# Performance work log

Measured on AMD Instinct MI355X. Metric: run time of the kernel, lower is better.

Reference implementation:

```python
import jax, jax.numpy as jnp
import numpy as np

DIM = 256
NUM_HEADS = 8
CHUNK = 64
EPS = 1e-5


def layernorm(x, g, b):
    m = jnp.mean(x, axis=-1, keepdims=True)
    v = jnp.mean((x - m) ** 2, axis=-1, keepdims=True)
    return (x - m) / jnp.sqrt(v + EPS) * g + b


def setup_inputs() -> dict:
    key = jax.random.key(0)
    ks = jax.random.split(key, 12)
    B, C, H, W = 8, DIM, 64, 64
    s = 1.0 / np.sqrt(C)
    return {
        "x": jax.random.normal(ks[0], (B, C, H, W), jnp.float32),
        "CVA_input": jax.random.normal(ks[1], (B, C, H, W), jnp.float32),
        "qn_g": jnp.ones((C,), jnp.float32), "qn_b": jnp.zeros((C,), jnp.float32),
        "kn_g": jnp.ones((C,), jnp.float32), "kn_b": jnp.zeros((C,), jnp.float32),
        "vn_g": jnp.ones((C,), jnp.float32), "vn_b": jnp.zeros((C,), jnp.float32),
        "Wq": jax.random.normal(ks[2], (C, C), jnp.float32) * s,
        "bq": jnp.zeros((C,), jnp.float32),
        "Wk": jax.random.normal(ks[3], (C, C), jnp.float32) * s,
        "bk": jnp.zeros((C,), jnp.float32),
        "Wv": jax.random.normal(ks[4], (C, C), jnp.float32) * s,
        "bv": jnp.zeros((C,), jnp.float32),
        "Wp": jax.random.normal(ks[5], (C, C), jnp.float32) * s,
        "bp": jnp.zeros((C,), jnp.float32),
    }


def reference(x, CVA_input, qn_g, qn_b, kn_g, kn_b, vn_g, vn_b,
              Wq, bq, Wk, bk, Wv, bv, Wp, bp):
    B, C, H, W = x.shape
    N = H * W
    nh = NUM_HEADS
    hd = C // nh
    scale = hd ** -0.5
    nc = N // CHUNK  # number of non-overlapping chunks

    xs = x.reshape(B, C, N).transpose(0, 2, 1)          # [B,N,C]
    cva = CVA_input.reshape(B, -1, C)                    # [B,N,C] (raw reshape, as in torch)

    def heads(t):  # [B,N,C] -> [B,nh,nc,CHUNK,hd]
        return t.reshape(B, N, nh, hd).transpose(0, 2, 1, 3).reshape(B, nh, nc, CHUNK, hd)

    q = heads(layernorm(cva, qn_g, qn_b) @ Wq + bq)
    k = heads(layernorm(cva, kn_g, kn_b) @ Wk + bk)
    v = heads(layernorm(xs, vn_g, vn_b) @ Wv + bv)

    # block-local attention: each chunk attends only within itself
    scores = jnp.einsum('bhncd,bhnkd->bhnck', q, k) * scale  # [B,nh,nc,CHUNK,CHUNK]
    probs = jax.nn.softmax(scores, axis=-1)
    o = jnp.einsum('bhnck,bhnkd->bhncd', probs, v)           # [B,nh,nc,CHUNK,hd]

    o = o.reshape(B, nh, N, hd).transpose(0, 2, 1, 3).reshape(B, N, C)
    out = o @ Wp + bp                                        # [B,N,C]
    return out.transpose(0, 2, 1).reshape(B, C, H, W)
```

## Files before the change

kernel.cpp:

```cpp
#include <hip/hip_runtime.h>
#include <hip/hip_bf16.h>

#define NTOK 4096
#define BATCH 8
#define NROWS (BATCH * NTOK)

typedef __attribute__((ext_vector_type(8))) short bfx8;
typedef __attribute__((ext_vector_type(4))) short bfx4;
typedef __attribute__((ext_vector_type(4))) float f32x4;

__device__ __forceinline__ short f2bf(float f) {
    unsigned u = __builtin_bit_cast(unsigned, f);
    u += 0x7fffu + ((u >> 16) & 1u);
    return (short)(u >> 16);
}
__device__ __forceinline__ unsigned pk2(float a, float b) {
    return (unsigned)(unsigned short)f2bf(a) | ((unsigned)(unsigned short)f2bf(b) << 16);
}

#define MFMA16(a, b, c) __builtin_amdgcn_mfma_f32_16x16x32_bf16(a, b, c, 0, 0, 0)
#define LGKM0()                                              \
    do {                                                     \
        asm volatile("s_waitcnt lgkmcnt(0)" ::: "memory");   \
        __builtin_amdgcn_sched_barrier(0);                   \
    } while (0)

__global__ __launch_bounds__(256) void prep_w(
    const float* __restrict__ Wq, const float* __restrict__ Wk,
    const float* __restrict__ Wv, const float* __restrict__ Wp,
    const float* __restrict__ qg, const float* __restrict__ qb,
    const float* __restrict__ kg, const float* __restrict__ kb,
    const float* __restrict__ vg, const float* __restrict__ vb,
    short* __restrict__ wt, float* __restrict__ bbp) {
    int m = blockIdx.x;
    int ci0 = blockIdx.y * 16;
    const float *W, *g, *be;
    float scale = 1.0f;
    if (m == 0)      { W = Wq; g = qg; be = qb; scale = 0.17677669529663687f; }
    else if (m == 1) { W = Wk; g = kg; be = kb; }
    else if (m == 2) { W = Wv; g = vg; be = vb; }
    else             { W = Wp; g = nullptr; be = nullptr; }
    __shared__ float tile[16][257];
    int t = threadIdx.x;
#pragma unroll
    for (int i = 0; i < 16; i++)
        tile[i][t] = W[(size_t)(ci0 + i) * 256 + t];
    __syncthreads();
    float p = 0.f;
    if (be) {
#pragma unroll
        for (int i = 0; i < 16; i++) p += be[ci0 + i] * tile[i][t];
    }
    bbp[(m * 16 + blockIdx.y) * 256 + t] = p;
    short* WT = wt + m * 65536 + t * 256 + ci0;
    bfx8 o0, o1;
#pragma unroll
    for (int j = 0; j < 8; j++) {
        float gv = g ? g[ci0 + j] : 1.0f;
        o0[j] = f2bf(scale * gv * tile[j][t]);
    }
#pragma unroll
    for (int j = 0; j < 8; j++) {
        float gv = g ? g[ci0 + 8 + j] : 1.0f;
        o1[j] = f2bf(scale * gv * tile[8 + j][t]);
    }
    *reinterpret_cast<bfx8*>(WT) = o0;
    *reinterpret_cast<bfx8*>(WT + 8) = o1;
}

__global__ __launch_bounds__(256) void prep_b(
    const float* __restrict__ bq, const float* __restrict__ bk,
    const float* __restrict__ bv, const float* __restrict__ bp,
    const float* __restrict__ bbp, float* __restrict__ bb) {
    int m = blockIdx.x, t = threadIdx.x;
    const float* bias = (m == 0) ? bq : (m == 1) ? bk : (m == 2) ? bv : bp;
    float scale = (m == 0) ? 0.17677669529663687f : 1.0f;
    float s = bias[t];
#pragma unroll
    for (int i = 0; i < 16; i++) s += bbp[(m * 16 + i) * 256 + t];
    bb[m * 256 + t] = scale * s;
}

__global__ __launch_bounds__(512, 4) void mega(const float* __restrict__ x,
                                               const float* __restrict__ cva,
                                               const short* __restrict__ wt,
                                               const float* __restrict__ bb,
                                               float* __restrict__ out) {
    int id = blockIdx.x;
    int b = id >> 6, ch = id & 63;
    int t = threadIdx.x, w = t >> 6, l = t & 63, c = l & 15, g = l >> 4;

    __shared__ short A[64 * 264];
    __shared__ short scr_[8][2560];
    __shared__ float red[8][64][2];
    short* S = scr_[w];

    const float* xb   = x + (size_t)b * 1048576 + ch * 64;
    const float* cvab = cva + (size_t)(b * 4096 + ch * 64) * 256;

    {
        float4 vv[8];
#pragma unroll
        for (int i = 0; i < 8; i++)
            vv[i] = *reinterpret_cast<const float4*>(cvab + (size_t)(w * 8 + i) * 256 + l * 4);
#pragma unroll
        for (int i = 0; i < 8; i++) {
            int row = w * 8 + i;
            float4 v = vv[i];
            float s = v.x + v.y + v.z + v.w;
            float q2 = v.x * v.x + v.y * v.y + v.z * v.z + v.w * v.w;
#pragma unroll
            for (int m = 1; m < 64; m <<= 1) { s += __shfl_xor(s, m); q2 += __shfl_xor(q2, m); }
            float mean = s * (1.0f / 256.0f);
            float rstd = rsqrtf(q2 * (1.0f / 256.0f) - mean * mean + 1e-5f);
            bfx4 o;
            o[0] = f2bf((v.x - mean) * rstd);
            o[1] = f2bf((v.y - mean) * rstd);
            o[2] = f2bf((v.z - mean) * rstd);
            o[3] = f2bf((v.w - mean) * rstd);
            *reinterpret_cast<bfx4*>(A + row * 264 + l * 4) = o;
        }
    }
    __syncthreads();

    f32x4 qa[4][2] = {}, ka[4][2] = {};
    {
        const short* wq0 = wt + (size_t)(w * 32 + c) * 256 + g * 8;
        const short* wq1 = wq0 + 16 * 256;
        const short* wk0 = wq0 + 65536;
        const short* wk1 = wq1 + 65536;
#pragma unroll
        for (int ks = 0; ks < 8; ks++) {
            bfx8 af[4];
#pragma unroll
            for (int m = 0; m < 4; m++)
                af[m] = *reinterpret_cast<const bfx8*>(A + (m * 16 + c) * 264 + ks * 32 + g * 8);
            bfx8 q0 = *reinterpret_cast<const bfx8*>(wq0 + ks * 32);
            bfx8 q1 = *reinterpret_cast<const bfx8*>(wq1 + ks * 32);
            bfx8 k0 = *reinterpret_cast<const bfx8*>(wk0 + ks * 32);
            bfx8 k1 = *reinterpret_cast<const bfx8*>(wk1 + ks * 32);
#pragma unroll
            for (int m = 0; m < 4; m++) {
                qa[m][0] = MFMA16(af[m], q0, qa[m][0]);
                qa[m][1] = MFMA16(af[m], q1, qa[m][1]);
                ka[m][0] = MFMA16(af[m], k0, ka[m][0]);
                ka[m][1] = MFMA16(af[m], k1, ka[m][1]);
            }
        }
    }

    float xg[32];
#pragma unroll
    for (int i = 0; i < 32; i++) xg[i] = xb[(size_t)(w * 32 + i) * 4096 + l];

    bfx8 qf[4];
    {
        float b0 = bb[w * 32 + c], b1 = bb[w * 32 + 16 + c];
#pragma unroll
        for (int m = 0; m < 4; m++)
#pragma unroll
            for (int j = 0; j < 4; j++) {
                S[(m * 16 + g * 4 + j) * 40 + c]      = f2bf(qa[m][0][j] + b0);
                S[(m * 16 + g * 4 + j) * 40 + 16 + c] = f2bf(qa[m][1][j] + b1);
            }
        LGKM0();
#pragma unroll
        for (int np = 0; np < 4; np++)
            qf[np] = *reinterpret_cast<const bfx8*>(S + (np * 16 + c) * 40 + g * 8);
        LGKM0();
    }

    bfx8 kf[4];
    {
        float b0 = bb[256 + w * 32 + c], b1 = bb[256 + w * 32 + 16 + c];
#pragma unroll
        for (int m = 0; m < 4; m++)
#pragma unroll
            for (int j = 0; j < 4; j++) {
                S[(m * 16 + g * 4 + j) * 40 + c]      = f2bf(ka[m][0][j] + b0);
                S[(m * 16 + g * 4 + j) * 40 + 16 + c] = f2bf(ka[m][1][j] + b1);
            }
        LGKM0();
#pragma unroll
        for (int m = 0; m < 4; m++)
            kf[m] = *reinterpret_cast<const bfx8*>(S + (m * 16 + c) * 40 + g * 8);
        LGKM0();
    }

    {
        float s = 0.f, q2 = 0.f;
#pragma unroll
        for (int i = 0; i < 32; i++) { s += xg[i]; q2 += xg[i] * xg[i]; }
        red[w][l][0] = s;
        red[w][l][1] = q2;
    }
    __syncthreads();

    float xmean, xrstd;
    {
        float s = 0.f, q2 = 0.f;
#pragma unroll
        for (int j2 = 0; j2 < 8; j2++) { s += red[j2][l][0]; q2 += red[j2][l][1]; }
        xmean = s * (1.0f / 256.0f);
        xrstd = rsqrtf(q2 * (1.0f / 256.0f) - xmean * xmean + 1e-5f);
    }

#pragma unroll
    for (int i2 = 0; i2 < 4; i2++) {
        bfx8 o;
#pragma unroll
        for (int jj = 0; jj < 8; jj++) o[jj] = f2bf((xg[i2 * 8 + jj] - xmean) * xrstd);
        *reinterpret_cast<bfx8*>(A + l * 264 + w * 32 + i2 * 8) = o;
    }
    __syncthreads();

    f32x4 va[4][2] = {};
    {
        const short* w0 = wt + 2 * 65536 + (size_t)(w * 32 + c) * 256 + g * 8;
        const short* w1 = w0 + 16 * 256;
#pragma unroll
        for (int ks = 0; ks < 8; ks++) {
            bfx8 af[4];
#pragma unroll
            for (int m = 0; m < 4; m++)
                af[m] = *reinterpret_cast<const bfx8*>(A + (m * 16 + c) * 264 + ks * 32 + g * 8);
            bfx8 v0 = *reinterpret_cast<const bfx8*>(w0 + ks * 32);
            bfx8 v1 = *reinterpret_cast<const bfx8*>(w1 + ks * 32);
#pragma unroll
            for (int m = 0; m < 4; m++) {
                va[m][0] = MFMA16(af[m], v0, va[m][0]);
                va[m][1] = MFMA16(af[m], v1, va[m][1]);
            }
        }
    }

    f32x4 sa[4][4] = {};
#pragma unroll
    for (int m = 0; m < 4; m++)
#pragma unroll
        for (int np = 0; np < 4; np++)
            sa[m][np] = MFMA16(kf[m], qf[np], sa[m][np]);

    float rs[4];
#pragma unroll
    for (int np = 0; np < 4; np++) {
        float mx = sa[0][np][0];
#pragma unroll
        for (int m = 0; m < 4; m++)
#pragma unroll
            for (int j = 0; j < 4; j++) mx = fmaxf(mx, sa[m][np][j]);
        mx = fmaxf(mx, __shfl_xor(mx, 16));
        mx = fmaxf(mx, __shfl_xor(mx, 32));
        float sum = 0.f;
#pragma unroll
        for (int m = 0; m < 4; m++)
#pragma unroll
            for (int j = 0; j < 4; j++) {
                float e = __expf(sa[m][np][j] - mx);
                sa[m][np][j] = e;
                sum += e;
            }
        sum += __shfl_xor(sum, 16);
        sum += __shfl_xor(sum, 32);
        rs[np] = 1.0f / sum;
    }

    unsigned Pp[4][4][2];
#pragma unroll
    for (int m = 0; m < 4; m++)
#pragma unroll
        for (int np = 0; np < 4; np++) {
            Pp[m][np][0] = pk2(sa[m][np][0], sa[m][np][1]);
            Pp[m][np][1] = pk2(sa[m][np][2], sa[m][np][3]);
        }
    __syncthreads();

    bfx8 vf[2][2];
    {
        float b0 = bb[512 + w * 32 + c], b1 = bb[512 + w * 32 + 16 + c];
#pragma unroll
        for (int m = 0; m < 4; m++) {
            bfx4 t0, t1;
#pragma unroll
            for (int j = 0; j < 4; j++) {
                t0[j] = f2bf(va[m][0][j] + b0);
                t1[j] = f2bf(va[m][1][j] + b1);
            }
            *reinterpret_cast<bfx4*>(S + c * 72 + m * 16 + g * 4)        = t0;
            *reinterpret_cast<bfx4*>(S + (16 + c) * 72 + m * 16 + g * 4) = t1;
        }
        LGKM0();
#pragma unroll
        for (int ks = 0; ks < 2; ks++)
#pragma unroll
            for (int mD = 0; mD < 2; mD++)
                vf[ks][mD] = *reinterpret_cast<const bfx8*>(S + (mD * 16 + c) * 72 + ks * 32 + g * 8);
        LGKM0();
    }

    f32x4 oa[2][4] = {};
#pragma unroll
    for (int ks = 0; ks < 2; ks++) {
#pragma unroll
        for (int m2 = 0; m2 < 2; m2++)
#pragma unroll
            for (int np = 0; np < 4; np++) {
                *reinterpret_cast<unsigned*>(S + (np * 16 + c) * 40 + m2 * 16 + g * 4)     = Pp[ks * 2 + m2][np][0];
                *reinterpret_cast<unsigned*>(S + (np * 16 + c) * 40 + m2 * 16 + g * 4 + 2) = Pp[ks * 2 + m2][np][1];
            }
        LGKM0();
        bfx8 pf[4];
#pragma unroll
        for (int np = 0; np < 4; np++)
            pf[np] = *reinterpret_cast<const bfx8*>(S + (np * 16 + c) * 40 + g * 8);
        LGKM0();
#pragma unroll
        for (int mD = 0; mD < 2; mD++)
#pragma unroll
            for (int np = 0; np < 4; np++)
                oa[mD][np] = MFMA16(vf[ks][mD], pf[np], oa[mD][np]);
    }

#pragma unroll
    for (int mD = 0; mD < 2; mD++)
#pragma unroll
        for (int np = 0; np < 4; np++) {
            bfx4 o4;
#pragma unroll
            for (int j = 0; j < 4; j++) o4[j] = f2bf(oa[mD][np][j] * rs[np]);
            *reinterpret_cast<bfx4*>(A + (np * 16 + c) * 264 + w * 32 + mD * 16 + g * 4) = o4;
        }
    __syncthreads();

    {
        f32x4 pa[4][2] = {};
        const short* w0 = wt + 3 * 65536 + (size_t)(w * 32 + c) * 256 + g * 8;
        const short* w1 = w0 + 16 * 256;
#pragma unroll
        for (int ks = 0; ks < 8; ks++) {
            bfx8 af[4];
#pragma unroll
            for (int m = 0; m < 4; m++)
                af[m] = *reinterpret_cast<const bfx8*>(A + (m * 16 + c) * 264 + ks * 32 + g * 8);
            bfx8 p0 = *reinterpret_cast<const bfx8*>(w0 + ks * 32);
            bfx8 p1 = *reinterpret_cast<const bfx8*>(w1 + ks * 32);
#pragma unroll
            for (int m = 0; m < 4; m++) {
                pa[m][0] = MFMA16(af[m], p0, pa[m][0]);
                pa[m][1] = MFMA16(af[m], p1, pa[m][1]);
            }
        }
        float* trw = reinterpret_cast<float*>(S);
        float* outb = out + (size_t)b * 1048576 + ch * 64;
#pragma unroll
        for (int p = 0; p < 2; p++) {
            float bvv = bb[768 + w * 32 + p * 16 + c];
#pragma unroll
            for (int m = 0; m < 4; m++)
#pragma unroll
                for (int j = 0; j < 4; j++)
                    trw[c * 65 + m * 16 + g * 4 + j] = pa[m][p][j] + bvv;
            LGKM0();
#pragma unroll
            for (int cl = 0; cl < 16; cl++) {
                int co = w * 32 + p * 16 + cl;
                outb[(size_t)co * 4096 + l] = trw[cl * 65 + l];
            }
            LGKM0();
        }
    }
}

extern "C" void kernel_launch(void* const* d_in, const int* in_sizes, int n_in,
                              void* d_out, int out_size, void* d_ws, size_t ws_size,
                              hipStream_t stream) {
    const float* x   = (const float*)d_in[0];
    const float* cva = (const float*)d_in[1];
    const float* qg  = (const float*)d_in[2];
    const float* qb  = (const float*)d_in[3];
    const float* kg  = (const float*)d_in[4];
    const float* kb  = (const float*)d_in[5];
    const float* vg  = (const float*)d_in[6];
    const float* vb  = (const float*)d_in[7];
    const float* Wq  = (const float*)d_in[8];
    const float* bq  = (const float*)d_in[9];
    const float* Wk  = (const float*)d_in[10];
    const float* bk  = (const float*)d_in[11];
    const float* Wv  = (const float*)d_in[12];
    const float* bv  = (const float*)d_in[13];
    const float* Wp  = (const float*)d_in[14];
    const float* bp  = (const float*)d_in[15];
    float* out = (float*)d_out;
    char* ws = (char*)d_ws;

    short* wt  = (short*)(ws);
    float* bb  = (float*)(ws + 4 * 65536 * sizeof(short));
    float* bbp = bb + 1024;

    prep_w<<<dim3(4, 16), 256, 0, stream>>>(Wq, Wk, Wv, Wp, qg, qb, kg, kb, vg, vb,
                                            wt, bbp);
    prep_b<<<4, 256, 0, stream>>>(bq, bk, bv, bp, bbp, bb);

    mega<<<512, 512, 0, stream>>>(x, cva, wt, bb, out);
}
```

Baseline: 70.92 us.

## Restructure cva LayerNorm loads, hoist softmax before V GEMM, store output directly

The cva LayerNorm now has each lane load 16 contiguous floats of a row, with four rows per wavefront reduced over 16 lanes, so the shuffle reduction is shorter and LDS writes are wider. The QK^T scores and softmax move ahead of the V projection GEMM, which may let the exp work overlap with the MFMA stream. The final projection drops its LDS transpose and writes float4 stores straight from the MFMA accumulator layout, removing LDS traffic and two waits. The direct stores are 16-byte segments spread across channels rather than fully coalesced 256-byte rows, and holding more values live may raise register pressure.

Result: faster. 67.08 us (-5.4%).

```diff
diff --git a/kernel.cpp b/kernel.cpp
--- a/kernel.cpp
+++ b/kernel.cpp
@@ -99,26 +99,44 @@
     const float* cvab = cva + (size_t)(b * 4096 + ch * 64) * 256;
 
     {
-        float4 vv[8];
-#pragma unroll
-        for (int i = 0; i < 8; i++)
-            vv[i] = *reinterpret_cast<const float4*>(cvab + (size_t)(w * 8 + i) * 256 + l * 4);
-#pragma unroll
-        for (int i = 0; i < 8; i++) {
-            int row = w * 8 + i;
-            float4 v = vv[i];
-            float s = v.x + v.y + v.z + v.w;
-            float q2 = v.x * v.x + v.y * v.y + v.z * v.z + v.w * v.w;
-#pragma unroll
-            for (int m = 1; m < 64; m <<= 1) { s += __shfl_xor(s, m); q2 += __shfl_xor(q2, m); }
+        int r16 = l >> 4;
+        float fv[2][16];
+#pragma unroll
+        for (int p2 = 0; p2 < 2; p2++) {
+            int row = w * 8 + p2 * 4 + r16;
+#pragma unroll
+            for (int i = 0; i < 4; i++) {
+                float4 v4 = *reinterpret_cast<const float4*>(
+                    cvab + (size_t)row * 256 + c * 16 + i * 4);
+                fv[p2][i * 4 + 0] = v4.x;
+                fv[p2][i * 4 + 1] = v4.y;
+                fv[p2][i * 4 + 2] = v4.z;
+                fv[p2][i * 4 + 3] = v4.w;
+            }
+        }
+#pragma unroll
+        for (int p2 = 0; p2 < 2; p2++) {
+            int row = w * 8 + p2 * 4 + r16;
+            float s = 0.f, q2 = 0.f;
+#pragma unroll
+            for (int i = 0; i < 16; i++) {
+                s += fv[p2][i];
+                q2 += fv[p2][i] * fv[p2][i];
+            }
+            s += __shfl_xor(s, 1);  q2 += __shfl_xor(q2, 1);
+            s += __shfl_xor(s, 2);  q2 += __shfl_xor(q2, 2);
+            s += __shfl_xor(s, 4);  q2 += __shfl_xor(q2, 4);
+            s += __shfl_xor(s, 8);  q2 += __shfl_xor(q2, 8);
             float mean = s * (1.0f / 256.0f);
             float rstd = rsqrtf(q2 * (1.0f / 256.0f) - mean * mean + 1e-5f);
-            bfx4 o;
-            o[0] = f2bf((v.x - mean) * rstd);
-            o[1] = f2bf((v.y - mean) * rstd);
-            o[2] = f2bf((v.z - mean) * rstd);
-            o[3] = f2bf((v.w - mean) * rstd);
-            *reinterpret_cast<bfx4*>(A + row * 264 + l * 4) = o;
+            bfx8 o0, o1;
+#pragma unroll
+            for (int jj = 0; jj < 8; jj++) {
+                o0[jj] = f2bf((fv[p2][jj] - mean) * rstd);
+                o1[jj] = f2bf((fv[p2][8 + jj] - mean) * rstd);
+            }
+            *reinterpret_cast<bfx8*>(A + row * 264 + c * 16) = o0;
+            *reinterpret_cast<bfx8*>(A + row * 264 + c * 16 + 8) = o1;
         }
     }
     __syncthreads();
@@ -214,6 +232,46 @@
     }
     __syncthreads();
 
+    f32x4 sa[4][4] = {};
+#pragma unroll
+    for (int m = 0; m < 4; m++)
+#pragma unroll
+        for (int np = 0; np < 4; np++)
+            sa[m][np] = MFMA16(kf[m], qf[np], sa[m][np]);
+
+    float rs[4];
+#pragma unroll
+    for (int np = 0; np < 4; np++) {
+        float mx = sa[0][np][0];
+#pragma unroll
+        for (int m = 0; m < 4; m++)
+#pragma unroll
+            for (int j = 0; j < 4; j++) mx = fmaxf(mx, sa[m][np][j]);
+        mx = fmaxf(mx, __shfl_xor(mx, 16));
+        mx = fmaxf(mx, __shfl_xor(mx, 32));
+        float sum = 0.f;
+#pragma unroll
+        for (int m = 0; m < 4; m++)
+#pragma unroll
+            for (int j = 0; j < 4; j++) {
+                float e = __expf(sa[m][np][j] - mx);
+                sa[m][np][j] = e;
+                sum += e;
+            }
+        sum += __shfl_xor(sum, 16);
+        sum += __shfl_xor(sum, 32);
+        rs[np] = 1.0f / sum;
+    }
+
+    unsigned Pp[4][4][2];
+#pragma unroll
+    for (int m = 0; m < 4; m++)
+#pragma unroll
+        for (int np = 0; np < 4; np++) {
+            Pp[m][np][0] = pk2(sa[m][np][0], sa[m][np][1]);
+            Pp[m][np][1] = pk2(sa[m][np][2], sa[m][np][3]);
+        }
+
     f32x4 va[4][2] = {};
     {
         const short* w0 = wt + 2 * 65536 + (size_t)(w * 32 + c) * 256 + g * 8;
@@ -233,46 +291,6 @@
             }
         }
     }
-
-    f32x4 sa[4][4] = {};
-#pragma unroll
-    for (int m = 0; m < 4; m++)
-#pragma unroll
-        for (int np = 0; np < 4; np++)
-            sa[m][np] = MFMA16(kf[m], qf[np], sa[m][np]);
-
-    float rs[4];
-#pragma unroll
-    for (int np = 0; np < 4; np++) {
-        float mx = sa[0][np][0];
-#pragma unroll
-        for (int m = 0; m < 4; m++)
-#pragma unroll
-            for (int j = 0; j < 4; j++) mx = fmaxf(mx, sa[m][np][j]);
-        mx = fmaxf(mx, __shfl_xor(mx, 16));
-        mx = fmaxf(mx, __shfl_xor(mx, 32));
-        float sum = 0.f;
-#pragma unroll
-        for (int m = 0; m < 4; m++)
-#pragma unroll
-            for (int j = 0; j < 4; j++) {
-                float e = __expf(sa[m][np][j] - mx);
-                sa[m][np][j] = e;
-                sum += e;
-            }
-        sum += __shfl_xor(sum, 16);
-        sum += __shfl_xor(sum, 32);
-        rs[np] = 1.0f / sum;
-    }
-
-    unsigned Pp[4][4][2];
-#pragma unroll
-    for (int m = 0; m < 4; m++)
-#pragma unroll
-        for (int np = 0; np < 4; np++) {
-            Pp[m][np][0] = pk2(sa[m][np][0], sa[m][np][1]);
-            Pp[m][np][1] = pk2(sa[m][np][2], sa[m][np][3]);
-        }
     __syncthreads();
 
     bfx8 vf[2][2];
@@ -350,23 +368,21 @@
                 pa[m][1] = MFMA16(af[m], p1, pa[m][1]);
             }
         }
-        float* trw = reinterpret_cast<float*>(S);
         float* outb = out + (size_t)b * 1048576 + ch * 64;
 #pragma unroll
         for (int p = 0; p < 2; p++) {
-            float bvv = bb[768 + w * 32 + p * 16 + c];
-#pragma unroll
-            for (int m = 0; m < 4; m++)
-#pragma unroll
-                for (int j = 0; j < 4; j++)
-                    trw[c * 65 + m * 16 + g * 4 + j] = pa[m][p][j] + bvv;
-            LGKM0();
-#pragma unroll
-            for (int cl = 0; cl < 16; cl++) {
-                int co = w * 32 + p * 16 + cl;
-                outb[(size_t)co * 4096 + l] = trw[cl * 65 + l];
-            }
-            LGKM0();
+            int co = w * 32 + p * 16 + c;
+            float bvv = bb[768 + co];
+            float* op = outb + (size_t)co * 4096 + g * 4;
+#pragma unroll
+            for (int m = 0; m < 4; m++) {
+                float4 st;
+                st.x = pa[m][p][0] + bvv;
+                st.y = pa[m][p][1] + bvv;
+                st.z = pa[m][p][2] + bvv;
+                st.w = pa[m][p][3] + bvv;
+                *reinterpret_cast<float4*>(op + m * 16) = st;
+            }
         }
     }
 }
```
